# Optimization experiments

Hardware: AMD Instinct MI355X
Metric: run time of the kernel (lower is better)

Reference implementation:

```python
import jax, jax.numpy as jnp
import numpy as np

NEG_BIG = -9e15

def setup_inputs() -> dict:
    key = jax.random.key(0)
    k1, k2, k3, k4 = jax.random.split(key, 4)
    N, Fin, Fout = 8192, 128, 64
    x = jax.random.normal(k1, (N, Fin), dtype=jnp.float32)
    adj = jax.random.randint(k2, (N, N), 0, 2).astype(jnp.float32)
    W = jax.random.normal(k3, (Fin, Fout), dtype=jnp.float32) * (1.0 / np.sqrt(Fin))
    a = jax.random.normal(k4, (2 * Fout, 1), dtype=jnp.float32) * (1.0 / np.sqrt(2 * Fout))
    return {"x": x, "adj": adj, "W": W, "a": a}

def reference(x, adj, W, a):
    Fout = W.shape[1]
    Wh = x @ W                              # [N, Fout]
    Wh1 = Wh @ a[:Fout, :]                  # [N, 1]
    Wh2 = Wh @ a[Fout:, :]                  # [N, 1]
    e = jax.nn.leaky_relu(Wh1 + Wh2.T, negative_slope=0.2)  # [N, N]
    attention = jnp.where(adj > 0, e, NEG_BIG)
    attention = jax.nn.softmax(attention, axis=1)
    # dropout is identity in eval mode (training=False)
    h_prime = attention @ Wh                # [N, Fout]
    return jax.nn.elu(h_prime)
```

## Files before the change

### kernel.cpp

```cpp
#include <hip/hip_runtime.h>
#include <cstdint>
#include <cstddef>


#define NN   8192
#define FIN  128
#define FOUT 64
#define SJ   16
#define JCHUNK (NN / SJ)

typedef __attribute__((ext_vector_type(8))) short   short8;
typedef __attribute__((ext_vector_type(4))) float   f32x4;

#define LOG2E 1.44269504088896340736f
#define NTL(p) __builtin_nontemporal_load((const f32x4*)(p))

__global__ __launch_bounds__(256) void gat_phaseA(
    const float* __restrict__ x, const float* __restrict__ W,
    const float* __restrict__ a, unsigned short* __restrict__ WhP,
    float* __restrict__ Wh1, float* __restrict__ Wh2)
{
  const int wid  = threadIdx.x >> 6;
  const int lane = threadIdx.x & 63;
  const int row0 = (blockIdx.x * 4 + wid) * 4;
  const float a1 = a[lane];
  const float a2 = a[FOUT + lane];
  float acc[4] = {0.f, 0.f, 0.f, 0.f};
#pragma unroll 4
  for (int k = 0; k < FIN; k += 4) {
    float4 wv0 = make_float4(W[(k+0)*FOUT + lane], W[(k+1)*FOUT + lane],
                             W[(k+2)*FOUT + lane], W[(k+3)*FOUT + lane]);
#pragma unroll
    for (int r = 0; r < 4; ++r) {
      float4 xv = *(const float4*)(x + (row0 + r) * FIN + k);
      acc[r] = fmaf(xv.x, wv0.x, acc[r]);
      acc[r] = fmaf(xv.y, wv0.y, acc[r]);
      acc[r] = fmaf(xv.z, wv0.z, acc[r]);
      acc[r] = fmaf(xv.w, wv0.w, acc[r]);
    }
  }
  const int ft = lane >> 4, m = lane & 15;
#pragma unroll
  for (int r = 0; r < 4; ++r) {
    const int row = row0 + r;
    unsigned int u = __float_as_uint(acc[r]);
    unsigned int rb = (u + 0x7FFFu + ((u >> 16) & 1u)) >> 16;
    const int B0 = row >> 5, qq = (row >> 3) & 3, e = row & 7;
    WhP[(size_t)(B0 * 4 + ft) * 512 + (qq * 16 + m) * 8 + e] = (unsigned short)rb;
    float s1 = acc[r] * a1, s2 = acc[r] * a2;
#pragma unroll
    for (int off = 32; off; off >>= 1) {
      s1 += __shfl_xor(s1, off);
      s2 += __shfl_xor(s2, off);
    }
    if (lane == 0) { Wh1[row] = s1 * LOG2E; Wh2[row] = s2 * LOG2E; }
  }
}

#define AF_ONE(AF, AD0, AD1, W20, W21, WH1, RS)                          \
    _Pragma("unroll")                                                    \
    for (int e = 0; e < 4; ++e) {                                        \
      float t0 = (WH1) + (W20)[e];                                       \
      t0 = fmaxf(t0, 0.2f * t0);              \
      float p0 = exp2f(t0) * (AD0)[e];         \
      unsigned int pu0 = __float_as_uint(p0) & 0xFFFF0000u;              \
      RS += __uint_as_float(pu0);            \
      AF[e] = (short)(pu0 >> 16);                                        \
      float t1 = (WH1) + (W21)[e];                                       \
      t1 = fmaxf(t1, 0.2f * t1);                                         \
      float p1 = exp2f(t1) * (AD1)[e];                                   \
      unsigned int pu1 = __float_as_uint(p1) & 0xFFFF0000u;              \
      RS += __uint_as_float(pu1);                                        \
      AF[4 + e] = (short)(pu1 >> 16);                                    \
    }

#define GAT_BODY(AD00, AD01, AD10, AD11, BLK, JPF)                       \
  {                                                                      \
    const unsigned short* pb = panel + (BLK) * 2048 + lane * 8;          \
    short8 b0 = *(const short8*)(pb);                                    \
    short8 b1 = *(const short8*)(pb + 512);                              \
    short8 b2 = *(const short8*)(pb + 1024);                             \
    short8 b3 = *(const short8*)(pb + 1536);                             \
    const float* wp = w2lds + (BLK) * 32 + q * 8;                        \
    f32x4 w20 = *(const f32x4*)(wp);                                     \
    f32x4 w21 = *(const f32x4*)(wp + 4);                                 \
    short8 af0, af1;                                                     \
    AF_ONE(af0, AD00, AD01, w20, w21, wh1_0, rsum0);                     \
    AF_ONE(af1, AD10, AD11, w20, w21, wh1_1, rsum1);                     \
    AD00 = NTL(adjrow0 + (JPF)); AD01 = NTL(adjrow0 + (JPF) + 4);        \
    AD10 = NTL(adjrow1 + (JPF)); AD11 = NTL(adjrow1 + (JPF) + 4);        \
    c00 = __builtin_amdgcn_mfma_f32_16x16x32_bf16(af0, b0, c00, 0,0,0);  \
    c01 = __builtin_amdgcn_mfma_f32_16x16x32_bf16(af0, b1, c01, 0,0,0);  \
    c02 = __builtin_amdgcn_mfma_f32_16x16x32_bf16(af0, b2, c02, 0,0,0);  \
    c03 = __builtin_amdgcn_mfma_f32_16x16x32_bf16(af0, b3, c03, 0,0,0);  \
    c10 = __builtin_amdgcn_mfma_f32_16x16x32_bf16(af1, b0, c10, 0,0,0);  \
    c11 = __builtin_amdgcn_mfma_f32_16x16x32_bf16(af1, b1, c11, 0,0,0);  \
    c12 = __builtin_amdgcn_mfma_f32_16x16x32_bf16(af1, b2, c12, 0,0,0);  \
    c13 = __builtin_amdgcn_mfma_f32_16x16x32_bf16(af1, b3, c13, 0,0,0);  \
  }

__global__ __launch_bounds__(256, 2) void gat_phaseB(
    const float* __restrict__ adj, const unsigned short* __restrict__ WhP,
    const float* __restrict__ Wh1, const float* __restrict__ Wh2,
    float* __restrict__ accbuf, float* __restrict__ denbuf, int nslices)
{
  const int wid  = threadIdx.x >> 6;
  const int lane = threadIdx.x & 63;
  const int jc   = blockIdx.x % SJ;
  const int rg   = (blockIdx.x / SJ) * 4 + wid;
  const int m = lane & 15;
  const int q = lane >> 4;
  const int r0 = rg * 32 + m;
  const int r1 = r0 + 16;
  const float wh1_0 = Wh1[r0];
  const float wh1_1 = Wh1[r1];
  const float* adjrow0 = adj + (size_t)r0 * NN + q * 8;
  const float* adjrow1 = adj + (size_t)r1 * NN + q * 8;

  const int jbeg = jc * JCHUNK;

  f32x4 aS00, aS01, aS10, aS11;
  f32x4 bS00, bS01, bS10, bS11;
  f32x4 cS00, cS01, cS10, cS11;
  f32x4 dS00, dS01, dS10, dS11;
  aS00 = NTL(adjrow0 + jbeg);       aS01 = NTL(adjrow0 + jbeg + 4);
  aS10 = NTL(adjrow1 + jbeg);       aS11 = NTL(adjrow1 + jbeg + 4);
  bS00 = NTL(adjrow0 + jbeg + 32);  bS01 = NTL(adjrow0 + jbeg + 36);
  bS10 = NTL(adjrow1 + jbeg + 32);  bS11 = NTL(adjrow1 + jbeg + 36);
  cS00 = NTL(adjrow0 + jbeg + 64);  cS01 = NTL(adjrow0 + jbeg + 68);
  cS10 = NTL(adjrow1 + jbeg + 64);  cS11 = NTL(adjrow1 + jbeg + 68);
  dS00 = NTL(adjrow0 + jbeg + 96);  dS01 = NTL(adjrow0 + jbeg + 100);
  dS10 = NTL(adjrow1 + jbeg + 96);  dS11 = NTL(adjrow1 + jbeg + 100);

  __shared__ __align__(16) unsigned short panel[16 * 2048];
  __shared__ __align__(16) float w2lds[JCHUNK];
  {
    const f32x4* src = (const f32x4*)(WhP + (size_t)jc * 16 * 2048) + threadIdx.x;
    f32x4* dst = (f32x4*)panel + threadIdx.x;
#pragma unroll
    for (int k = 0; k < 16; ++k)
      dst[k * 256] = src[k * 256];
    if (threadIdx.x < JCHUNK / 4)
      ((f32x4*)w2lds)[threadIdx.x] =
          ((const f32x4*)(Wh2 + jbeg))[threadIdx.x];
  }
  __syncthreads();

  f32x4 c00 = {0.f,0.f,0.f,0.f}, c01 = c00, c02 = c00, c03 = c00;
  f32x4 c10 = c00, c11 = c00, c12 = c00, c13 = c00;
  float rsum0 = 0.f, rsum1 = 0.f;

#pragma unroll
  for (int bb = 0; bb < 16; bb += 4) {
    GAT_BODY(aS00, aS01, aS10, aS11, bb,     jbeg + ((bb + 4) & 15) * 32);
    GAT_BODY(bS00, bS01, bS10, bS11, bb + 1, jbeg + ((bb + 5) & 15) * 32);
    GAT_BODY(cS00, cS01, cS10, cS11, bb + 2, jbeg + ((bb + 6) & 15) * 32);
    GAT_BODY(dS00, dS01, dS10, dS11, bb + 3, jbeg + ((bb + 7) & 15) * 32);
  }

  rsum0 += __shfl_xor(rsum0, 16);
  rsum0 += __shfl_xor(rsum0, 32);
  rsum1 += __shfl_xor(rsum1, 16);
  rsum1 += __shfl_xor(rsum1, 32);

  const int slice = (nslices > 1) ? jc : 0;
  float* accout = accbuf + (size_t)slice * (NN * FOUT);
  float* denout = denbuf + slice * NN;
  f32x4 cc0[4] = {c00, c01, c02, c03};
  f32x4 cc1[4] = {c10, c11, c12, c13};
  if (nslices > 1) {
    if (q == 0) { denout[r0] = rsum0; denout[r1] = rsum1; }
#pragma unroll
    for (int ft = 0; ft < 4; ++ft)
#pragma unroll
      for (int r = 0; r < 4; ++r) {
        accout[(rg * 32 +      q * 4 + r) * FOUT + ft * 16 + m] = cc0[ft][r];
        accout[(rg * 32 + 16 + q * 4 + r) * FOUT + ft * 16 + m] = cc1[ft][r];
      }
  } else {
    if (q == 0) { atomicAdd(&denout[r0], rsum0); atomicAdd(&denout[r1], rsum1); }
#pragma unroll
    for (int ft = 0; ft < 4; ++ft)
#pragma unroll
      for (int r = 0; r < 4; ++r) {
        atomicAdd(&accout[(rg * 32 +      q * 4 + r) * FOUT + ft * 16 + m], cc0[ft][r]);
        atomicAdd(&accout[(rg * 32 + 16 + q * 4 + r) * FOUT + ft * 16 + m], cc1[ft][r]);
      }
  }
}

__global__ __launch_bounds__(256) void gat_phaseC(
    const float* __restrict__ accbuf, const float* __restrict__ denbuf,
    float* __restrict__ out, int nslices)
{
  const int idx4 = blockIdx.x * 256 + threadIdx.x;
  const int idx  = idx4 * 4;
  const int row  = idx >> 6;
  f32x4 s = {0.f, 0.f, 0.f, 0.f};
  float d = 0.f;
  for (int sl = 0; sl < nslices; ++sl) {
    f32x4 v = *(const f32x4*)(accbuf + (size_t)sl * (NN * FOUT) + idx);
    s += v;
    d += denbuf[sl * NN + row];
  }
  float inv = 1.0f / d;
  f32x4 o;
#pragma unroll
  for (int e = 0; e < 4; ++e) {
    float v = s[e] * inv;
    o[e] = (v > 0.f) ? v : expm1f(v);
  }
  *(f32x4*)(out + idx) = o;
}

extern "C" void kernel_launch(void* const* d_in, const int* in_sizes, int n_in,
                              void* d_out, int out_size, void* d_ws, size_t ws_size,
                              hipStream_t stream)
{
  const float* x   = (const float*)d_in[0];
  const float* adj = (const float*)d_in[1];
  const float* W   = (const float*)d_in[2];
  const float* a   = (const float*)d_in[3];
  float* out = (float*)d_out;

  const size_t accEl = (size_t)NN * FOUT;
  const size_t whpBytes = (size_t)(NN / 32) * 4 * 512 * 2;
  const size_t roomyBytes = (size_t)SJ * accEl * 4 + (size_t)SJ * NN * 4
                          + (size_t)NN * 8 + whpBytes;
  const int nslices = (ws_size >= roomyBytes) ? SJ : 1;

  char* ws = (char*)d_ws;
  float* accbuf = (float*)ws;
  size_t off = (size_t)nslices * accEl * 4;
  float* denbuf = (float*)(ws + off); off += (size_t)nslices * NN * 4;
  float* Wh1 = (float*)(ws + off);    off += (size_t)NN * 4;
  float* Wh2 = (float*)(ws + off);    off += (size_t)NN * 4;
  unsigned short* WhP = (unsigned short*)(ws + off);

  if (nslices == 1)
    hipMemsetAsync(accbuf, 0, accEl * 4 + (size_t)NN * 4, stream);

  gat_phaseA<<<NN / 16, 256, 0, stream>>>(x, W, a, WhP, Wh1, Wh2);
  gat_phaseB<<<((NN / 32) * SJ) / 4, 256, 0, stream>>>(adj, WhP, Wh1, Wh2,
                                                       accbuf, denbuf, nslices);
  gat_phaseC<<<(NN * FOUT) / 4 / 256, 256, 0, stream>>>(accbuf, denbuf, out, nslices);
}
```

Measured before the change: 377.2 us.

## Restructure adj prefetch into double-buffered 128-column bursts with sched barriers

Replaces the rolling per-block adjacency prefetch (four blocks ahead, issued inside each compute step) with two register buffers of four blocks each, loaded in bursts of 16 nontemporal loads. Sched barriers pin each burst between compute groups so more loads are in flight at once while the other buffer is consumed. It also drops the wasted wrap-around prefetches of the old loop. The cost is roughly double the prefetch register footprint (64 VGPRs of adj data), which may cause spills or lower occupancy under launch_bounds(256,2).

```diff
diff --git a/kernel.cpp b/kernel.cpp
--- a/kernel.cpp
+++ b/kernel.cpp
@@ -74,7 +74,7 @@
       AF[4 + e] = (short)(pu1 >> 16);                                    \
     }
 
-#define GAT_BODY(AD00, AD01, AD10, AD11, BLK, JPF)                       \
+#define GAT_BODY(AD00, AD01, AD10, AD11, BLK)                            \
   {                                                                      \
     const unsigned short* pb = panel + (BLK) * 2048 + lane * 8;          \
     short8 b0 = *(const short8*)(pb);                                    \
@@ -87,8 +87,6 @@
     short8 af0, af1;                                                     \
     AF_ONE(af0, AD00, AD01, w20, w21, wh1_0, rsum0);                     \
     AF_ONE(af1, AD10, AD11, w20, w21, wh1_1, rsum1);                     \
-    AD00 = NTL(adjrow0 + (JPF)); AD01 = NTL(adjrow0 + (JPF) + 4);        \
-    AD10 = NTL(adjrow1 + (JPF)); AD11 = NTL(adjrow1 + (JPF) + 4);        \
     c00 = __builtin_amdgcn_mfma_f32_16x16x32_bf16(af0, b0, c00, 0,0,0);  \
     c01 = __builtin_amdgcn_mfma_f32_16x16x32_bf16(af0, b1, c01, 0,0,0);  \
     c02 = __builtin_amdgcn_mfma_f32_16x16x32_bf16(af0, b2, c02, 0,0,0);  \
@@ -98,6 +96,16 @@
     c12 = __builtin_amdgcn_mfma_f32_16x16x32_bf16(af1, b2, c12, 0,0,0);  \
     c13 = __builtin_amdgcn_mfma_f32_16x16x32_bf16(af1, b3, c13, 0,0,0);  \
   }
+
+#define ADJ_BURST(P0,P1,P2,P3, Q0,Q1,Q2,Q3, R0,R1,R2,R3, S0,S1,S2,S3, J)\
+    P0 = NTL(adjrow0 + (J));        P1 = NTL(adjrow0 + (J) + 4);         \
+    Q0 = NTL(adjrow0 + (J) + 32);   Q1 = NTL(adjrow0 + (J) + 36);        \
+    R0 = NTL(adjrow0 + (J) + 64);   R1 = NTL(adjrow0 + (J) + 68);        \
+    S0 = NTL(adjrow0 + (J) + 96);   S1 = NTL(adjrow0 + (J) + 100);       \
+    P2 = NTL(adjrow1 + (J));        P3 = NTL(adjrow1 + (J) + 4);         \
+    Q2 = NTL(adjrow1 + (J) + 32);   Q3 = NTL(adjrow1 + (J) + 36);        \
+    R2 = NTL(adjrow1 + (J) + 64);   R3 = NTL(adjrow1 + (J) + 68);        \
+    S2 = NTL(adjrow1 + (J) + 96);   S3 = NTL(adjrow1 + (J) + 100);
 
 __global__ __launch_bounds__(256, 2) void gat_phaseB(
     const float* __restrict__ adj, const unsigned short* __restrict__ WhP,
@@ -119,18 +127,13 @@
 
   const int jbeg = jc * JCHUNK;
 
-  f32x4 aS00, aS01, aS10, aS11;
-  f32x4 bS00, bS01, bS10, bS11;
-  f32x4 cS00, cS01, cS10, cS11;
-  f32x4 dS00, dS01, dS10, dS11;
-  aS00 = NTL(adjrow0 + jbeg);       aS01 = NTL(adjrow0 + jbeg + 4);
-  aS10 = NTL(adjrow1 + jbeg);       aS11 = NTL(adjrow1 + jbeg + 4);
-  bS00 = NTL(adjrow0 + jbeg + 32);  bS01 = NTL(adjrow0 + jbeg + 36);
-  bS10 = NTL(adjrow1 + jbeg + 32);  bS11 = NTL(adjrow1 + jbeg + 36);
-  cS00 = NTL(adjrow0 + jbeg + 64);  cS01 = NTL(adjrow0 + jbeg + 68);
-  cS10 = NTL(adjrow1 + jbeg + 64);  cS11 = NTL(adjrow1 + jbeg + 68);
-  dS00 = NTL(adjrow0 + jbeg + 96);  dS01 = NTL(adjrow0 + jbeg + 100);
-  dS10 = NTL(adjrow1 + jbeg + 96);  dS11 = NTL(adjrow1 + jbeg + 100);
+  f32x4 pA0,pA1,pA2,pA3, pB0,pB1,pB2,pB3, pC0,pC1,pC2,pC3, pD0,pD1,pD2,pD3;
+  f32x4 pE0,pE1,pE2,pE3, pF0,pF1,pF2,pF3, pG0,pG1,pG2,pG3, pH0,pH1,pH2,pH3;
+
+  ADJ_BURST(pA0,pA1,pA2,pA3, pB0,pB1,pB2,pB3, pC0,pC1,pC2,pC3,
+            pD0,pD1,pD2,pD3, jbeg);
+  ADJ_BURST(pE0,pE1,pE2,pE3, pF0,pF1,pF2,pF3, pG0,pG1,pG2,pG3,
+            pH0,pH1,pH2,pH3, jbeg + 128);
 
   __shared__ __align__(16) unsigned short panel[16 * 2048];
   __shared__ __align__(16) float w2lds[JCHUNK];
@@ -150,13 +153,30 @@
   f32x4 c10 = c00, c11 = c00, c12 = c00, c13 = c00;
   float rsum0 = 0.f, rsum1 = 0.f;
 
-#pragma unroll
-  for (int bb = 0; bb < 16; bb += 4) {
-    GAT_BODY(aS00, aS01, aS10, aS11, bb,     jbeg + ((bb + 4) & 15) * 32);
-    GAT_BODY(bS00, bS01, bS10, bS11, bb + 1, jbeg + ((bb + 5) & 15) * 32);
-    GAT_BODY(cS00, cS01, cS10, cS11, bb + 2, jbeg + ((bb + 6) & 15) * 32);
-    GAT_BODY(dS00, dS01, dS10, dS11, bb + 3, jbeg + ((bb + 7) & 15) * 32);
-  }
+  GAT_BODY(pA0, pA1, pA2, pA3, 0);
+  GAT_BODY(pB0, pB1, pB2, pB3, 1);
+  GAT_BODY(pC0, pC1, pC2, pC3, 2);
+  GAT_BODY(pD0, pD1, pD2, pD3, 3);
+  __builtin_amdgcn_sched_barrier(0);
+  ADJ_BURST(pA0,pA1,pA2,pA3, pB0,pB1,pB2,pB3, pC0,pC1,pC2,pC3,
+            pD0,pD1,pD2,pD3, jbeg + 256);
+  __builtin_amdgcn_sched_barrier(0);
+  GAT_BODY(pE0, pE1, pE2, pE3, 4);
+  GAT_BODY(pF0, pF1, pF2, pF3, 5);
+  GAT_BODY(pG0, pG1, pG2, pG3, 6);
+  GAT_BODY(pH0, pH1, pH2, pH3, 7);
+  __builtin_amdgcn_sched_barrier(0);
+  ADJ_BURST(pE0,pE1,pE2,pE3, pF0,pF1,pF2,pF3, pG0,pG1,pG2,pG3,
+            pH0,pH1,pH2,pH3, jbeg + 384);
+  __builtin_amdgcn_sched_barrier(0);
+  GAT_BODY(pA0, pA1, pA2, pA3, 8);
+  GAT_BODY(pB0, pB1, pB2, pB3, 9);
+  GAT_BODY(pC0, pC1, pC2, pC3, 10);
+  GAT_BODY(pD0, pD1, pD2, pD3, 11);
+  GAT_BODY(pE0, pE1, pE2, pE3, 12);
+  GAT_BODY(pF0, pF1, pF2, pF3, 13);
+  GAT_BODY(pG0, pG1, pG2, pG3, 14);
+  GAT_BODY(pH0, pH1, pH2, pH3, 15);
 
   rsum0 += __shfl_xor(rsum0, 16);
   rsum0 += __shfl_xor(rsum0, 32);
```

After: 379.8 us. No clear change (+0.7%).

## Process 64 rows per wave in GAT phase B to reuse the LDS panel

Applied to the files above, without the earlier changes.

Each wave now handles four 16-row strips (64 rows) instead of two, so every B fragment and Wh2 value read from LDS feeds twice as many MFMAs. The prefetch depth for adjacency drops from four blocks to two, but each stage now loads four rows. The grid halves to 512 blocks, which lowers the cost of loading the WhP panel into LDS per row but reduces parallelism and raises register pressure (32 accumulators plus 16 prefetch vectors), with a risk of spills or lower occupancy under launch_bounds(256,2).

```diff
diff --git a/kernel.cpp b/kernel.cpp
--- a/kernel.cpp
+++ b/kernel.cpp
@@ -74,7 +74,7 @@
       AF[4 + e] = (short)(pu1 >> 16);                                    \
     }
 
-#define GAT_BODY(AD00, AD01, AD10, AD11, BLK, JPF)                       \
+#define GAT_BODY(A00,A01, A10,A11, A20,A21, A30,A31, BLK, JPF)           \
   {                                                                      \
     const unsigned short* pb = panel + (BLK) * 2048 + lane * 8;          \
     short8 b0 = *(const short8*)(pb);                                    \
@@ -84,11 +84,15 @@
     const float* wp = w2lds + (BLK) * 32 + q * 8;                        \
     f32x4 w20 = *(const f32x4*)(wp);                                     \
     f32x4 w21 = *(const f32x4*)(wp + 4);                                 \
-    short8 af0, af1;                                                     \
-    AF_ONE(af0, AD00, AD01, w20, w21, wh1_0, rsum0);                     \
-    AF_ONE(af1, AD10, AD11, w20, w21, wh1_1, rsum1);                     \
-    AD00 = NTL(adjrow0 + (JPF)); AD01 = NTL(adjrow0 + (JPF) + 4);        \
-    AD10 = NTL(adjrow1 + (JPF)); AD11 = NTL(adjrow1 + (JPF) + 4);        \
+    short8 af0, af1, af2, af3;                                           \
+    AF_ONE(af0, A00, A01, w20, w21, wh1_0, rsum0);                       \
+    AF_ONE(af1, A10, A11, w20, w21, wh1_1, rsum1);                       \
+    AF_ONE(af2, A20, A21, w20, w21, wh1_2, rsum2);                       \
+    AF_ONE(af3, A30, A31, w20, w21, wh1_3, rsum3);                       \
+    A00 = NTL(adjrow0 + (JPF)); A01 = NTL(adjrow0 + (JPF) + 4);          \
+    A10 = NTL(adjrow1 + (JPF)); A11 = NTL(adjrow1 + (JPF) + 4);          \
+    A20 = NTL(adjrow2 + (JPF)); A21 = NTL(adjrow2 + (JPF) + 4);          \
+    A30 = NTL(adjrow3 + (JPF)); A31 = NTL(adjrow3 + (JPF) + 4);          \
     c00 = __builtin_amdgcn_mfma_f32_16x16x32_bf16(af0, b0, c00, 0,0,0);  \
     c01 = __builtin_amdgcn_mfma_f32_16x16x32_bf16(af0, b1, c01, 0,0,0);  \
     c02 = __builtin_amdgcn_mfma_f32_16x16x32_bf16(af0, b2, c02, 0,0,0);  \
@@ -97,6 +101,14 @@
     c11 = __builtin_amdgcn_mfma_f32_16x16x32_bf16(af1, b1, c11, 0,0,0);  \
     c12 = __builtin_amdgcn_mfma_f32_16x16x32_bf16(af1, b2, c12, 0,0,0);  \
     c13 = __builtin_amdgcn_mfma_f32_16x16x32_bf16(af1, b3, c13, 0,0,0);  \
+    c20 = __builtin_amdgcn_mfma_f32_16x16x32_bf16(af2, b0, c20, 0,0,0);  \
+    c21 = __builtin_amdgcn_mfma_f32_16x16x32_bf16(af2, b1, c21, 0,0,0);  \
+    c22 = __builtin_amdgcn_mfma_f32_16x16x32_bf16(af2, b2, c22, 0,0,0);  \
+    c23 = __builtin_amdgcn_mfma_f32_16x16x32_bf16(af2, b3, c23, 0,0,0);  \
+    c30 = __builtin_amdgcn_mfma_f32_16x16x32_bf16(af3, b0, c30, 0,0,0);  \
+    c31 = __builtin_amdgcn_mfma_f32_16x16x32_bf16(af3, b1, c31, 0,0,0);  \
+    c32 = __builtin_amdgcn_mfma_f32_16x16x32_bf16(af3, b2, c32, 0,0,0);  \
+    c33 = __builtin_amdgcn_mfma_f32_16x16x32_bf16(af3, b3, c33, 0,0,0);  \
   }
 
 __global__ __launch_bounds__(256, 2) void gat_phaseB(
@@ -110,27 +122,27 @@
   const int rg   = (blockIdx.x / SJ) * 4 + wid;
   const int m = lane & 15;
   const int q = lane >> 4;
-  const int r0 = rg * 32 + m;
-  const int r1 = r0 + 16;
-  const float wh1_0 = Wh1[r0];
-  const float wh1_1 = Wh1[r1];
+  const int r0 = rg * 64 + m;
+  const int r1 = r0 + 16, r2 = r0 + 32, r3 = r0 + 48;
+  const float wh1_0 = Wh1[r0], wh1_1 = Wh1[r1];
+  const float wh1_2 = Wh1[r2], wh1_3 = Wh1[r3];
   const float* adjrow0 = adj + (size_t)r0 * NN + q * 8;
   const float* adjrow1 = adj + (size_t)r1 * NN + q * 8;
+  const float* adjrow2 = adj + (size_t)r2 * NN + q * 8;
+  const float* adjrow3 = adj + (size_t)r3 * NN + q * 8;
 
   const int jbeg = jc * JCHUNK;
 
-  f32x4 aS00, aS01, aS10, aS11;
-  f32x4 bS00, bS01, bS10, bS11;
-  f32x4 cS00, cS01, cS10, cS11;
-  f32x4 dS00, dS01, dS10, dS11;
-  aS00 = NTL(adjrow0 + jbeg);       aS01 = NTL(adjrow0 + jbeg + 4);
-  aS10 = NTL(adjrow1 + jbeg);       aS11 = NTL(adjrow1 + jbeg + 4);
-  bS00 = NTL(adjrow0 + jbeg + 32);  bS01 = NTL(adjrow0 + jbeg + 36);
-  bS10 = NTL(adjrow1 + jbeg + 32);  bS11 = NTL(adjrow1 + jbeg + 36);
-  cS00 = NTL(adjrow0 + jbeg + 64);  cS01 = NTL(adjrow0 + jbeg + 68);
-  cS10 = NTL(adjrow1 + jbeg + 64);  cS11 = NTL(adjrow1 + jbeg + 68);
-  dS00 = NTL(adjrow0 + jbeg + 96);  dS01 = NTL(adjrow0 + jbeg + 100);
-  dS10 = NTL(adjrow1 + jbeg + 96);  dS11 = NTL(adjrow1 + jbeg + 100);
+  f32x4 aA00,aA01, aA10,aA11, aA20,aA21, aA30,aA31;
+  f32x4 aB00,aB01, aB10,aB11, aB20,aB21, aB30,aB31;
+  aA00 = NTL(adjrow0 + jbeg);      aA01 = NTL(adjrow0 + jbeg + 4);
+  aA10 = NTL(adjrow1 + jbeg);      aA11 = NTL(adjrow1 + jbeg + 4);
+  aA20 = NTL(adjrow2 + jbeg);      aA21 = NTL(adjrow2 + jbeg + 4);
+  aA30 = NTL(adjrow3 + jbeg);      aA31 = NTL(adjrow3 + jbeg + 4);
+  aB00 = NTL(adjrow0 + jbeg + 32); aB01 = NTL(adjrow0 + jbeg + 36);
+  aB10 = NTL(adjrow1 + jbeg + 32); aB11 = NTL(adjrow1 + jbeg + 36);
+  aB20 = NTL(adjrow2 + jbeg + 32); aB21 = NTL(adjrow2 + jbeg + 36);
+  aB30 = NTL(adjrow3 + jbeg + 32); aB31 = NTL(adjrow3 + jbeg + 36);
 
   __shared__ __align__(16) unsigned short panel[16 * 2048];
   __shared__ __align__(16) float w2lds[JCHUNK];
@@ -148,44 +160,54 @@
 
   f32x4 c00 = {0.f,0.f,0.f,0.f}, c01 = c00, c02 = c00, c03 = c00;
   f32x4 c10 = c00, c11 = c00, c12 = c00, c13 = c00;
-  float rsum0 = 0.f, rsum1 = 0.f;
-
-#pragma unroll
-  for (int bb = 0; bb < 16; bb += 4) {
-    GAT_BODY(aS00, aS01, aS10, aS11, bb,     jbeg + ((bb + 4) & 15) * 32);
-    GAT_BODY(bS00, bS01, bS10, bS11, bb + 1, jbeg + ((bb + 5) & 15) * 32);
-    GAT_BODY(cS00, cS01, cS10, cS11, bb + 2, jbeg + ((bb + 6) & 15) * 32);
-    GAT_BODY(dS00, dS01, dS10, dS11, bb + 3, jbeg + ((bb + 7) & 15) * 32);
-  }
-
-  rsum0 += __shfl_xor(rsum0, 16);
-  rsum0 += __shfl_xor(rsum0, 32);
-  rsum1 += __shfl_xor(rsum1, 16);
-  rsum1 += __shfl_xor(rsum1, 32);
+  f32x4 c20 = c00, c21 = c00, c22 = c00, c23 = c00;
+  f32x4 c30 = c00, c31 = c00, c32 = c00, c33 = c00;
+  float rsum0 = 0.f, rsum1 = 0.f, rsum2 = 0.f, rsum3 = 0.f;
+
+#pragma unroll
+  for (int bb = 0; bb < 16; bb += 2) {
+    GAT_BODY(aA00,aA01, aA10,aA11, aA20,aA21, aA30,aA31,
+             bb,     jbeg + ((bb + 2) & 15) * 32);
+    GAT_BODY(aB00,aB01, aB10,aB11, aB20,aB21, aB30,aB31,
+             bb + 1, jbeg + ((bb + 3) & 15) * 32);
+  }
+
+  rsum0 += __shfl_xor(rsum0, 16); rsum0 += __shfl_xor(rsum0, 32);
+  rsum1 += __shfl_xor(rsum1, 16); rsum1 += __shfl_xor(rsum1, 32);
+  rsum2 += __shfl_xor(rsum2, 16); rsum2 += __shfl_xor(rsum2, 32);
+  rsum3 += __shfl_xor(rsum3, 16); rsum3 += __shfl_xor(rsum3, 32);
 
   const int slice = (nslices > 1) ? jc : 0;
   float* accout = accbuf + (size_t)slice * (NN * FOUT);
   float* denout = denbuf + slice * NN;
-  f32x4 cc0[4] = {c00, c01, c02, c03};
-  f32x4 cc1[4] = {c10, c11, c12, c13};
+  f32x4 cc[4][4] = {{c00, c01, c02, c03}, {c10, c11, c12, c13},
+                    {c20, c21, c22, c23}, {c30, c31, c32, c33}};
+  float rs[4] = {rsum0, rsum1, rsum2, rsum3};
   if (nslices > 1) {
-    if (q == 0) { denout[r0] = rsum0; denout[r1] = rsum1; }
-#pragma unroll
-    for (int ft = 0; ft < 4; ++ft)
-#pragma unroll
-      for (int r = 0; r < 4; ++r) {
-        accout[(rg * 32 +      q * 4 + r) * FOUT + ft * 16 + m] = cc0[ft][r];
-        accout[(rg * 32 + 16 + q * 4 + r) * FOUT + ft * 16 + m] = cc1[ft][r];
-      }
+    if (q == 0) {
+#pragma unroll
+      for (int s = 0; s < 4; ++s) denout[r0 + s * 16] = rs[s];
+    }
+#pragma unroll
+    for (int s = 0; s < 4; ++s)
+#pragma unroll
+      for (int ft = 0; ft < 4; ++ft)
+#pragma unroll
+        for (int r = 0; r < 4; ++r)
+          accout[(rg * 64 + s * 16 + q * 4 + r) * FOUT + ft * 16 + m] = cc[s][ft][r];
   } else {
-    if (q == 0) { atomicAdd(&denout[r0], rsum0); atomicAdd(&denout[r1], rsum1); }
-#pragma unroll
-    for (int ft = 0; ft < 4; ++ft)
-#pragma unroll
-      for (int r = 0; r < 4; ++r) {
-        atomicAdd(&accout[(rg * 32 +      q * 4 + r) * FOUT + ft * 16 + m], cc0[ft][r]);
-        atomicAdd(&accout[(rg * 32 + 16 + q * 4 + r) * FOUT + ft * 16 + m], cc1[ft][r]);
-      }
+    if (q == 0) {
+#pragma unroll
+      for (int s = 0; s < 4; ++s) atomicAdd(&denout[r0 + s * 16], rs[s]);
+    }
+#pragma unroll
+    for (int s = 0; s < 4; ++s)
+#pragma unroll
+      for (int ft = 0; ft < 4; ++ft)
+#pragma unroll
+        for (int r = 0; r < 4; ++r)
+          atomicAdd(&accout[(rg * 64 + s * 16 + q * 4 + r) * FOUT + ft * 16 + m],
+                    cc[s][ft][r]);
   }
 }
 
@@ -241,7 +263,7 @@
     hipMemsetAsync(accbuf, 0, accEl * 4 + (size_t)NN * 4, stream);
 
   gat_phaseA<<<NN / 16, 256, 0, stream>>>(x, W, a, WhP, Wh1, Wh2);
-  gat_phaseB<<<((NN / 32) * SJ) / 4, 256, 0, stream>>>(adj, WhP, Wh1, Wh2,
+  gat_phaseB<<<((NN / 64) * SJ) / 4, 256, 0, stream>>>(adj, WhP, Wh1, Wh2,
                                                        accbuf, denbuf, nslices);
   gat_phaseC<<<(NN * FOUT) / 4 / 256, 256, 0, stream>>>(accbuf, denbuf, out, nslices);
 }
```

Result: no change. 373.4 us (-1.0%).
